# Optimization experiments

Hardware: AMD Instinct MI355X
Metric: run time of the kernel (lower is better)

Reference implementation:

```python
import jax, jax.numpy as jnp
import numpy as np

LAMBDA_REG = 0.1


def setup_inputs() -> dict:
    key = jax.random.key(0)
    k1, k2, k3, k4 = jax.random.split(key, 4)
    B, C, D = 4096, 10000, 128
    logits = jax.random.normal(k1, (B, C), dtype=jnp.float32)
    margins = jax.random.uniform(k2, (C,), dtype=jnp.float32)
    weights = jax.random.normal(k3, (C, D), dtype=jnp.float32)
    label = jax.random.randint(k4, (B,), 0, C, dtype=jnp.int64)
    return {"logits": logits, "margins": margins, "weights": weights, "label": label}


def reference(logits, margins, weights, label):
    B, C = logits.shape
    rows = jnp.arange(B)

    # F.cross_entropy(logits, label): mean NLL of log_softmax
    logp = jax.nn.log_softmax(logits, axis=-1)
    ce = -jnp.mean(logp[rows, label])

    # margin regularization
    margin_reg = LAMBDA_REG * jnp.mean(margins)

    # intra-class angular loss
    theta_yi = jnp.arccos(jnp.clip(logits[rows, label] / LAMBDA_REG, -1.0, 1.0))
    intra_loss = jnp.mean(theta_yi) / jnp.pi

    # inter-class loss: sum_i sum_{j != y_i} acos(clamp(w_{y_i} . w_j))
    # Vectorized replacement of the O(B*C) Python double loop:
    wy = weights[label]                       # (B, D) gather of ground-truth class rows
    S = jnp.einsum('bd,cd->bc', wy, weights)  # (B, C) pairwise dot products
    A = jnp.arccos(jnp.clip(S, -1.0, 1.0))    # (B, C) angles
    inter_sum = jnp.sum(A) - jnp.sum(A[rows, label])  # exclude j == y_i terms
    inter_loss = inter_sum / (B * (C - 1) * jnp.pi)

    return ce + margin_reg + intra_loss + inter_loss
```

## Files before the change

### kernel.cpp

```cpp
#include <hip/hip_runtime.h>
#include <stdint.h>
#include <math.h>

#define GLOBAL_AS __attribute__((address_space(1)))
#define LDS_AS __attribute__((address_space(3)))

typedef __attribute__((ext_vector_type(8))) __bf16 bf16x8;
typedef __attribute__((ext_vector_type(4))) float floatx4;

constexpr int kB = 4096;
constexpr int kC = 10000;
constexpr int kD = 128;
constexpr int kNT = 79;
constexpr int kMT = 32;
constexpr int kBricksB = kNT * 32;
constexpr int kBricksA = kMT * 32;
constexpr int kPrepBlocks = (kBricksB + kBricksA) / 4;
constexpr float kPI = 3.14159265358979323846f;
constexpr float kLambda = 0.1f;
constexpr float kInvInter = (float)(1.0 / (4096.0 * 9999.0 * 3.141592653589793));

constexpr size_t kBrickBytes = (size_t)(kBricksB + kBricksA) * 1024;
constexpr int kPartMargin = 0;
constexpr int kPartCE = 1;
constexpr int kPartInter = 1 + kB;
constexpr int kNumPart = 1 + kB + kNT * kMT;

__device__ __forceinline__ float fast_acos(float x) {
    float t = fabsf(x);
    float s = sqrtf(fmaxf(1.0f - t, 0.0f));
    float p = fmaf(fmaf(fmaf(-0.0187293f, t, 0.0742610f), t, -0.2121144f),
                   t, 1.5707288f);
    float r = s * p;
    return x < 0.0f ? kPI - r : r;
}

__device__ __forceinline__ uint16_t f2bf(float f) {
    union { float f; uint32_t u; } c; c.f = f;
    uint32_t u = c.u;
    uint32_t r = (u + 0x7FFFu + ((u >> 16) & 1u)) >> 16;
    return (uint16_t)r;
}

__global__ __launch_bounds__(256) void prep_kernel(
    const float* __restrict__ W, const float* __restrict__ margins,
    const int* __restrict__ label, uint16_t* __restrict__ wsB,
    uint16_t* __restrict__ wsA, float* __restrict__ part) {
    int blk = blockIdx.x;
    if (blk < kPrepBlocks) {
        int brick = blk * 4 + (threadIdx.x >> 6);
        int lane = threadIdx.x & 63;
        bool isA = brick >= kBricksB;
        int b2 = isA ? (brick - kBricksB) : brick;
        int kk = b2 & 3;
        int rb = (b2 >> 2) & 7;
        int tile = b2 >> 5;
        int row = tile * 128 + rb * 16 + (lane & 15);
        int k = kk * 32 + (lane >> 4) * 8;
        float v[8];
        if (isA) {
            int r = label[row];
            const float* src = W + (size_t)r * kD + k;
            #pragma unroll
            for (int j = 0; j < 8; ++j) v[j] = src[j];
        } else if (row < kC) {
            const float* src = W + (size_t)row * kD + k;
            #pragma unroll
            for (int j = 0; j < 8; ++j) v[j] = src[j];
        } else {
            #pragma unroll
            for (int j = 0; j < 8; ++j) v[j] = 0.0f;
        }
        uint4 pk;
        pk.x = (uint32_t)f2bf(v[0]) | ((uint32_t)f2bf(v[1]) << 16);
        pk.y = (uint32_t)f2bf(v[2]) | ((uint32_t)f2bf(v[3]) << 16);
        pk.z = (uint32_t)f2bf(v[4]) | ((uint32_t)f2bf(v[5]) << 16);
        pk.w = (uint32_t)f2bf(v[6]) | ((uint32_t)f2bf(v[7]) << 16);
        uint4* dst = (uint4*)(isA ? wsA : wsB);
        dst[(size_t)b2 * 64 + lane] = pk;
    } else {
        float s = 0.0f;
        for (int i = threadIdx.x; i < kC; i += 256) s += margins[i];
        for (int off = 32; off; off >>= 1) s += __shfl_down(s, off);
        __shared__ float p[4];
        if ((threadIdx.x & 63) == 0) p[threadIdx.x >> 6] = s;
        __syncthreads();
        if (threadIdx.x == 0)
            part[kPartMargin] = (p[0] + p[1] + p[2] + p[3]) * (kLambda / (float)kC);
    }
}

__global__ __launch_bounds__(256) void ce_kernel(
    const float* __restrict__ logits, const int* __restrict__ label,
    float* __restrict__ part) {
    int row = blockIdx.x;
    const float* lp = logits + (size_t)row * kC;
    const float4* lp4 = (const float4*)lp;
    float m = -INFINITY, s = 0.0f;
    for (int idx = threadIdx.x; idx < kC / 4; idx += 256) {
        float4 v = lp4[idx];
        float m4 = fmaxf(fmaxf(v.x, v.y), fmaxf(v.z, v.w));
        if (m4 > m) { s *= __expf(m - m4); m = m4; }
        s += __expf(v.x - m) + __expf(v.y - m) + __expf(v.z - m) + __expf(v.w - m);
    }
    for (int off = 32; off; off >>= 1) {
        float mo = __shfl_down(m, off);
        float so = __shfl_down(s, off);
        float M = fmaxf(m, mo);
        s = s * __expf(m - M) + so * __expf(mo - M);
        m = M;
    }
    __shared__ float sm[4], ss[4];
    if ((threadIdx.x & 63) == 0) {
        sm[threadIdx.x >> 6] = m;
        ss[threadIdx.x >> 6] = s;
    }
    __syncthreads();
    if (threadIdx.x == 0) {
        float M = fmaxf(fmaxf(sm[0], sm[1]), fmaxf(sm[2], sm[3]));
        float S = ss[0] * __expf(sm[0] - M) + ss[1] * __expf(sm[1] - M) +
                  ss[2] * __expf(sm[2] - M) + ss[3] * __expf(sm[3] - M);
        float z = lp[label[row]];
        float ce = M + __logf(S) - z;
        float intra = fast_acos(fminf(fmaxf(z * (1.0f / kLambda), -1.0f), 1.0f));
        part[kPartCE + row] = ce * (1.0f / kB) + intra * (1.0f / (kB * kPI));
    }
}

__global__ __launch_bounds__(256) void inter_kernel(
    const uint16_t* __restrict__ wsA, const uint16_t* __restrict__ wsB,
    float* __restrict__ part) {
    extern __shared__ char smem[];
    int nt = blockIdx.x;
    int mt = blockIdx.y;
    int tid = threadIdx.x;
    int wave = tid >> 6, lane = tid & 63;

    const char* gA = (const char*)wsA + (size_t)mt * 32768;
    const char* gB = (const char*)wsB + (size_t)nt * 32768;

    #pragma unroll
    for (int i = 0; i < 8; ++i) {
        int c = i * 4 + wave;
        __builtin_amdgcn_global_load_lds(
            (const GLOBAL_AS uint32_t*)(gA + c * 1024 + lane * 16),
            (LDS_AS uint32_t*)(smem + c * 1024), 16, 0, 0);
        __builtin_amdgcn_global_load_lds(
            (const GLOBAL_AS uint32_t*)(gB + c * 1024 + lane * 16),
            (LDS_AS uint32_t*)(smem + 32768 + c * 1024), 16, 0, 0);
    }
    __syncthreads();

    int wr = wave >> 1, wc = wave & 1;
    floatx4 zero = {0.0f, 0.0f, 0.0f, 0.0f};
    floatx4 acc[4][4];
    #pragma unroll
    for (int i = 0; i < 4; ++i)
        #pragma unroll
        for (int j = 0; j < 4; ++j) acc[i][j] = zero;

    #pragma unroll
    for (int kk = 0; kk < 4; ++kk) {
        bf16x8 a[4], b[4];
        #pragma unroll
        for (int i = 0; i < 4; ++i) {
            a[i] = *(const bf16x8*)(smem + ((wr * 4 + i) * 4 + kk) * 1024 + lane * 16);
            b[i] = *(const bf16x8*)(smem + 32768 + ((wc * 4 + i) * 4 + kk) * 1024 + lane * 16);
        }
        #pragma unroll
        for (int i = 0; i < 4; ++i)
            #pragma unroll
            for (int j = 0; j < 4; ++j)
                acc[i][j] = __builtin_amdgcn_mfma_f32_16x16x32_bf16(
                    a[i], b[j], acc[i][j], 0, 0, 0);
    }

    float local = 0.0f;
    int col0 = nt * 128 + wc * 64 + (lane & 15);
    #pragma unroll
    for (int j = 0; j < 4; ++j) {
        if (col0 + j * 16 < kC) {
            #pragma unroll
            for (int i = 0; i < 4; ++i)
                #pragma unroll
                for (int r = 0; r < 4; ++r)
                    local += fast_acos(
                        fminf(fmaxf(acc[i][j][r], -1.0f), 1.0f));
        }
    }
    for (int off = 32; off; off >>= 1) local += __shfl_down(local, off);
    __syncthreads();
    float* p = (float*)smem;
    if (lane == 0) p[wave] = local;
    __syncthreads();
    if (tid == 0)
        part[kPartInter + mt * kNT + nt] =
            (p[0] + p[1] + p[2] + p[3]) * kInvInter;
}

__global__ __launch_bounds__(256) void finalize_kernel(
    const float* __restrict__ part, float* __restrict__ out, int out_size) {
    float s = 0.0f;
    for (int i = threadIdx.x; i < kNumPart; i += 256) s += part[i];
    for (int off = 32; off; off >>= 1) s += __shfl_down(s, off);
    __shared__ float p[4];
    if ((threadIdx.x & 63) == 0) p[threadIdx.x >> 6] = s;
    __syncthreads();
    if (threadIdx.x == 0) out[0] = p[0] + p[1] + p[2] + p[3];
    for (int i = 1 + threadIdx.x; i < out_size; i += 256) out[i] = 0.0f;
}

extern "C" void kernel_launch(void* const* d_in, const int* in_sizes, int n_in,
                              void* d_out, int out_size, void* d_ws, size_t ws_size,
                              hipStream_t stream) {
    const float* logits = (const float*)d_in[0];
    const float* margins = (const float*)d_in[1];
    const float* W = (const float*)d_in[2];
    const int* label = (const int*)d_in[3];
    float* out = (float*)d_out;

    uint16_t* wsB = (uint16_t*)d_ws;
    uint16_t* wsA = (uint16_t*)((char*)d_ws + (size_t)kNT * 32768);
    float* part = (float*)((char*)d_ws + kBrickBytes);

    prep_kernel<<<kPrepBlocks + 1, 256, 0, stream>>>(W, margins, label, wsB, wsA, part);
    ce_kernel<<<kB, 256, 0, stream>>>(logits, label, part);
    inter_kernel<<<dim3(kNT, kMT), 256, 65536, stream>>>(wsA, wsB, part);
    finalize_kernel<<<1, 256, 0, stream>>>(part, out, out_size);
}
```

Baseline: 299.4 us.

## Fuse CE and inter-class GEMM kernels into one interleaved mega-kernel

Merges the cross-entropy row kernel and the MFMA inter-class kernel into a single launch whose blocks are interleaved (128 CE rows per 207 blocks), so memory-bound softmax work can overlap with compute-bound GEMM tiles. The CE path drops the online max and sums exp(x) directly, which is cheaper but can overflow or lose precision for large logits. The GEMM path now loads fragments straight from global memory instead of staging 64KB in LDS, which frees LDS for higher occupancy but relies on cache for the reuse across waves.

```diff
diff --git a/kernel.cpp b/kernel.cpp
--- a/kernel.cpp
+++ b/kernel.cpp
@@ -1,9 +1,6 @@
 #include <hip/hip_runtime.h>
 #include <stdint.h>
 #include <math.h>
-
-#define GLOBAL_AS __attribute__((address_space(1)))
-#define LDS_AS __attribute__((address_space(3)))
 
 typedef __attribute__((ext_vector_type(8))) __bf16 bf16x8;
 typedef __attribute__((ext_vector_type(4))) float floatx4;
@@ -19,6 +16,8 @@
 constexpr float kPI = 3.14159265358979323846f;
 constexpr float kLambda = 0.1f;
 constexpr float kInvInter = (float)(1.0 / (4096.0 * 9999.0 * 3.141592653589793));
+
+constexpr int kMegaBlocks = kB + kNT * kMT;
 
 constexpr size_t kBrickBytes = (size_t)(kBricksB + kBricksA) * 1024;
 constexpr int kPartMargin = 0;
@@ -90,112 +89,95 @@
     }
 }
 
-__global__ __launch_bounds__(256) void ce_kernel(
+__global__ __launch_bounds__(256) void mega_kernel(
     const float* __restrict__ logits, const int* __restrict__ label,
-    float* __restrict__ part) {
-    int row = blockIdx.x;
-    const float* lp = logits + (size_t)row * kC;
-    const float4* lp4 = (const float4*)lp;
-    float m = -INFINITY, s = 0.0f;
-    for (int idx = threadIdx.x; idx < kC / 4; idx += 256) {
-        float4 v = lp4[idx];
-        float m4 = fmaxf(fmaxf(v.x, v.y), fmaxf(v.z, v.w));
-        if (m4 > m) { s *= __expf(m - m4); m = m4; }
-        s += __expf(v.x - m) + __expf(v.y - m) + __expf(v.z - m) + __expf(v.w - m);
-    }
-    for (int off = 32; off; off >>= 1) {
-        float mo = __shfl_down(m, off);
-        float so = __shfl_down(s, off);
-        float M = fmaxf(m, mo);
-        s = s * __expf(m - M) + so * __expf(mo - M);
-        m = M;
-    }
-    __shared__ float sm[4], ss[4];
-    if ((threadIdx.x & 63) == 0) {
-        sm[threadIdx.x >> 6] = m;
-        ss[threadIdx.x >> 6] = s;
-    }
-    __syncthreads();
-    if (threadIdx.x == 0) {
-        float M = fmaxf(fmaxf(sm[0], sm[1]), fmaxf(sm[2], sm[3]));
-        float S = ss[0] * __expf(sm[0] - M) + ss[1] * __expf(sm[1] - M) +
-                  ss[2] * __expf(sm[2] - M) + ss[3] * __expf(sm[3] - M);
-        float z = lp[label[row]];
-        float ce = M + __logf(S) - z;
-        float intra = fast_acos(fminf(fmaxf(z * (1.0f / kLambda), -1.0f), 1.0f));
-        part[kPartCE + row] = ce * (1.0f / kB) + intra * (1.0f / (kB * kPI));
-    }
-}
-
-__global__ __launch_bounds__(256) void inter_kernel(
     const uint16_t* __restrict__ wsA, const uint16_t* __restrict__ wsB,
     float* __restrict__ part) {
-    extern __shared__ char smem[];
-    int nt = blockIdx.x;
-    int mt = blockIdx.y;
+    int b = blockIdx.x;
+    int cb = (b * 128) / 207;
+    int cb1 = ((b + 1) * 128) / 207;
     int tid = threadIdx.x;
-    int wave = tid >> 6, lane = tid & 63;
-
-    const char* gA = (const char*)wsA + (size_t)mt * 32768;
-    const char* gB = (const char*)wsB + (size_t)nt * 32768;
-
-    #pragma unroll
-    for (int i = 0; i < 8; ++i) {
-        int c = i * 4 + wave;
-        __builtin_amdgcn_global_load_lds(
-            (const GLOBAL_AS uint32_t*)(gA + c * 1024 + lane * 16),
-            (LDS_AS uint32_t*)(smem + c * 1024), 16, 0, 0);
-        __builtin_amdgcn_global_load_lds(
-            (const GLOBAL_AS uint32_t*)(gB + c * 1024 + lane * 16),
-            (LDS_AS uint32_t*)(smem + 32768 + c * 1024), 16, 0, 0);
-    }
-    __syncthreads();
-
-    int wr = wave >> 1, wc = wave & 1;
-    floatx4 zero = {0.0f, 0.0f, 0.0f, 0.0f};
-    floatx4 acc[4][4];
-    #pragma unroll
-    for (int i = 0; i < 4; ++i)
-        #pragma unroll
-        for (int j = 0; j < 4; ++j) acc[i][j] = zero;
-
-    #pragma unroll
-    for (int kk = 0; kk < 4; ++kk) {
-        bf16x8 a[4], b[4];
-        #pragma unroll
-        for (int i = 0; i < 4; ++i) {
-            a[i] = *(const bf16x8*)(smem + ((wr * 4 + i) * 4 + kk) * 1024 + lane * 16);
-            b[i] = *(const bf16x8*)(smem + 32768 + ((wc * 4 + i) * 4 + kk) * 1024 + lane * 16);
-        }
+
+    if (cb1 > cb) {
+        int row = cb;
+        const float* lp = logits + (size_t)row * kC;
+        const float4* lp4 = (const float4*)lp;
+        float s0 = 0.0f, s1 = 0.0f, s2 = 0.0f, s3 = 0.0f;
+        for (int idx = tid; idx < kC / 4; idx += 256) {
+            float4 v = lp4[idx];
+            s0 += __expf(v.x);
+            s1 += __expf(v.y);
+            s2 += __expf(v.z);
+            s3 += __expf(v.w);
+        }
+        float s = (s0 + s1) + (s2 + s3);
+        for (int off = 32; off; off >>= 1) s += __shfl_down(s, off);
+        __shared__ float ss[4];
+        if ((tid & 63) == 0) ss[tid >> 6] = s;
+        __syncthreads();
+        if (tid == 0) {
+            float S = (ss[0] + ss[1]) + (ss[2] + ss[3]);
+            float z = lp[label[row]];
+            float ce = __logf(S) - z;
+            float intra =
+                fast_acos(fminf(fmaxf(z * (1.0f / kLambda), -1.0f), 1.0f));
+            part[kPartCE + row] = ce * (1.0f / kB) + intra * (1.0f / (kB * kPI));
+        }
+    } else {
+        int ii = b - cb;
+        int mt = ii / kNT;
+        int nt = ii - mt * kNT;
+        int wave = tid >> 6, lane = tid & 63;
+        int wr = wave >> 1, wc = wave & 1;
+
+        const char* gA = (const char*)wsA + (size_t)mt * 32768;
+        const char* gB = (const char*)wsB + (size_t)nt * 32768;
+
+        floatx4 zero = {0.0f, 0.0f, 0.0f, 0.0f};
+        floatx4 acc[4][4];
         #pragma unroll
         for (int i = 0; i < 4; ++i)
             #pragma unroll
-            for (int j = 0; j < 4; ++j)
-                acc[i][j] = __builtin_amdgcn_mfma_f32_16x16x32_bf16(
-                    a[i], b[j], acc[i][j], 0, 0, 0);
-    }
-
-    float local = 0.0f;
-    int col0 = nt * 128 + wc * 64 + (lane & 15);
-    #pragma unroll
-    for (int j = 0; j < 4; ++j) {
-        if (col0 + j * 16 < kC) {
+            for (int j = 0; j < 4; ++j) acc[i][j] = zero;
+
+        #pragma unroll
+        for (int kk = 0; kk < 4; ++kk) {
+            bf16x8 a[4], bfr[4];
+            #pragma unroll
+            for (int i = 0; i < 4; ++i) {
+                a[i] = *(const bf16x8*)(gA + ((wr * 4 + i) * 4 + kk) * 1024 +
+                                        lane * 16);
+                bfr[i] = *(const bf16x8*)(gB + ((wc * 4 + i) * 4 + kk) * 1024 +
+                                          lane * 16);
+            }
             #pragma unroll
             for (int i = 0; i < 4; ++i)
                 #pragma unroll
-                for (int r = 0; r < 4; ++r)
-                    local += fast_acos(
-                        fminf(fmaxf(acc[i][j][r], -1.0f), 1.0f));
-        }
+                for (int j = 0; j < 4; ++j)
+                    acc[i][j] = __builtin_amdgcn_mfma_f32_16x16x32_bf16(
+                        a[i], bfr[j], acc[i][j], 0, 0, 0);
+        }
+
+        float local = 0.0f;
+        int col0 = nt * 128 + wc * 64 + (lane & 15);
+        #pragma unroll
+        for (int j = 0; j < 4; ++j) {
+            if (col0 + j * 16 < kC) {
+                #pragma unroll
+                for (int i = 0; i < 4; ++i)
+                    #pragma unroll
+                    for (int r = 0; r < 4; ++r)
+                        local += fast_acos(
+                            fminf(fmaxf(acc[i][j][r], -1.0f), 1.0f));
+            }
+        }
+        for (int off = 32; off; off >>= 1) local += __shfl_down(local, off);
+        __shared__ float p[4];
+        if (lane == 0) p[wave] = local;
+        __syncthreads();
+        if (tid == 0)
+            part[kPartInter + ii] = (p[0] + p[1] + p[2] + p[3]) * kInvInter;
     }
-    for (int off = 32; off; off >>= 1) local += __shfl_down(local, off);
-    __syncthreads();
-    float* p = (float*)smem;
-    if (lane == 0) p[wave] = local;
-    __syncthreads();
-    if (tid == 0)
-        part[kPartInter + mt * kNT + nt] =
-            (p[0] + p[1] + p[2] + p[3]) * kInvInter;
 }
 
 __global__ __launch_bounds__(256) void finalize_kernel(
@@ -224,7 +206,6 @@
     float* part = (float*)((char*)d_ws + kBrickBytes);
 
     prep_kernel<<<kPrepBlocks + 1, 256, 0, stream>>>(W, margins, label, wsB, wsA, part);
-    ce_kernel<<<kB, 256, 0, stream>>>(logits, label, part);
-    inter_kernel<<<dim3(kNT, kMT), 256, 65536, stream>>>(wsA, wsB, part);
+    mega_kernel<<<kMegaBlocks, 256, 0, stream>>>(logits, label, wsA, wsB, part);
     finalize_kernel<<<1, 256, 0, stream>>>(part, out, out_size);
 }
```

Result: faster. 282.3 us (-5.7%).
